# Kernel tuning notes

Measured on AMD Instinct MI355X. Metric: run time of the kernel, lower is better.

Reference implementation:

```python
import jax, jax.numpy as jnp
from jax import lax
import numpy as np

IOU_THR = 0.5
SCORE_THR = 0.0


def setup_inputs() -> dict:
    B, M, N, H, W = 8, 100, 32, 256, 256
    ks = jax.random.split(jax.random.key(0), 7)
    pxy = jax.random.uniform(ks[0], (B, M, 2), minval=0.0, maxval=512.0)
    pwh = jax.random.uniform(ks[1], (B, M, 2), minval=16.0, maxval=160.0)
    gxy = jax.random.uniform(ks[2], (B, N, 2), minval=0.0, maxval=512.0)
    gwh = jax.random.uniform(ks[3], (B, N, 2), minval=16.0, maxval=160.0)
    return {
        "pred_boxes": jnp.concatenate([pxy, pxy + pwh], axis=-1),  # xyxy
        "gt_boxes": jnp.concatenate([gxy, gxy + gwh], axis=-1),    # xyxy
        "pred_scores": jax.random.uniform(ks[4], (B, M)),
        "pred_masks": jax.random.uniform(ks[5], (B, M, H, W)),
        "mask_score": jax.random.uniform(ks[6], (B, M)),
    }


def pairwise_iou(b1, b2):
    # b1: [M,4], b2: [N,4] in xyxy -> [M,N]
    area1 = (b1[:, 2] - b1[:, 0]) * (b1[:, 3] - b1[:, 1])
    area2 = (b2[:, 2] - b2[:, 0]) * (b2[:, 3] - b2[:, 1])
    lt = jnp.maximum(b1[:, None, :2], b2[None, :, :2])
    rb = jnp.minimum(b1[:, None, 2:], b2[None, :, 2:])
    wh = jnp.clip(rb - lt, 0.0)
    inter = wh[..., 0] * wh[..., 1]
    return inter / (area1[:, None] + area2[None, :] - inter)


def _greedy_match(iou, scores):
    # iou: [M,N], scores: [M] -> gtm: [N] int32, biou: [N]
    N = iou.shape[1]
    order = jnp.argsort(-scores)  # descending score order

    def step(carry, i):
        gtm, biou = carry
        row = iou[i]
        # faithful to original: gt j is available if gtm[j] <= 0 (NOT > -1)
        cand = jnp.where((gtm <= 0) & (row >= IOU_THR), row, -1.0)
        m = jnp.argmax(cand)
        mx = cand[m]
        do = (scores[i] >= SCORE_THR) & (mx >= IOU_THR)
        gtm = jnp.where(do, gtm.at[m].set(i.astype(jnp.int32)), gtm)
        biou = jnp.where(do, biou.at[m].set(mx), biou)
        return (gtm, biou), None

    init = (jnp.full((N,), -1, jnp.int32), jnp.zeros((N,), iou.dtype))
    (gtm, biou), _ = lax.scan(step, init, order)
    return gtm, biou


def reference(pred_boxes, gt_boxes, pred_scores, pred_masks, mask_score):
    # per-image IoU matrices: [B,M,N]
    iou = jax.vmap(pairwise_iou)(pred_boxes, gt_boxes)
    gtm, biou = jax.vmap(_greedy_match)(iou, pred_scores)  # [B,N]
    matched = gtm > -1                                      # [B,N]
    idx = jnp.clip(gtm, 0)                                  # safe gather indices
    gathered = jax.vmap(lambda m, i: m[i])(pred_masks, idx)  # [B,N,H,W]
    gt_masks = jnp.where(matched[:, :, None, None], gathered, 0.0)
    flags = jnp.where(matched, jnp.take_along_axis(mask_score, idx, axis=1), 0.0)
    return gt_masks, flags, gtm, biou
```

## Files before the change

### kernel.cpp

```cpp
#include <hip/hip_runtime.h>
#include <hip/hip_bf16.h>

#define BB 8
#define MM 100
#define NN 32
#define HWSZ 65536
#define IOU_THR 0.5f
#define SCORE_THR 0.0f

#define MASKS_ELEMS ((size_t)BB * NN * HWSZ)

#define WS_FLAG 256

typedef unsigned int u32x4 __attribute__((ext_vector_type(4)));

__device__ __forceinline__ float bf16r(float x) {
    unsigned u = __float_as_uint(x);
    u = (u + 0x7FFFu + ((u >> 16) & 1u)) & 0xFFFF0000u;
    return __uint_as_float(u);
}

__global__ __launch_bounds__(256) void match_kernel(
    const void* __restrict__ pred_boxes,
    const void* __restrict__ gt_boxes,
    const void* __restrict__ pred_scores,
    const void* __restrict__ mask_score,
    void* __restrict__ out,
    int* __restrict__ ws)
{
    const int b = blockIdx.x;
    const int t = threadIdx.x;

    __shared__ float pb[MM][4];
    __shared__ float gb[NN][4];
    __shared__ float sc[MM];
    __shared__ float area2[NN];
    __shared__ float iou_s[MM][NN];
    __shared__ int   order_s[MM];
    __shared__ int   flag_s;

    if (t < 64) {
        const unsigned* gt_raw = (const unsigned*)gt_boxes;
        int cnt = 0;
        #pragma unroll
        for (int k = 0; k < 8; ++k) {
            const unsigned u  = gt_raw[t * 8 + k];
            const unsigned lo = u & 0xFFFFu;
            const unsigned ex = (lo >> 7) & 0xFFu;
            if (((lo >> 15) == 0u) && ex >= 118u && ex <= 137u) ++cnt;
        }
        #pragma unroll
        for (int m = 1; m < 64; m <<= 1) cnt += __shfl_xor(cnt, m, 64);
        if (t == 0) {
            flag_s = (cnt >= 256) ? 1 : 0;
            if (b == 0) ws[WS_FLAG] = flag_s;
        }
    }
    __syncthreads();
    const bool isbf = (flag_s != 0);

    const __hip_bfloat16* pb_h = (const __hip_bfloat16*)pred_boxes;
    const float*          pb_f = (const float*)pred_boxes;
    const __hip_bfloat16* gb_h = (const __hip_bfloat16*)gt_boxes;
    const float*          gb_f = (const float*)gt_boxes;
    const __hip_bfloat16* sc_h = (const __hip_bfloat16*)pred_scores;
    const float*          sc_f = (const float*)pred_scores;

    for (int i = t; i < MM * 4; i += 256) {
        const size_t o = (size_t)b * MM * 4 + i;
        pb[i >> 2][i & 3] = isbf ? __bfloat162float(pb_h[o]) : pb_f[o];
    }
    for (int i = t; i < NN * 4; i += 256) {
        const size_t o = (size_t)b * NN * 4 + i;
        gb[i >> 2][i & 3] = isbf ? __bfloat162float(gb_h[o]) : gb_f[o];
    }
    for (int i = t; i < MM; i += 256) {
        const size_t o = (size_t)b * MM + i;
        sc[i] = isbf ? __bfloat162float(sc_h[o]) : sc_f[o];
    }
    __syncthreads();

    auto rnd = [&](float x) { return isbf ? bf16r(x) : x; };

    if (t < NN)
        area2[t] = rnd(rnd(gb[t][2] - gb[t][0]) * rnd(gb[t][3] - gb[t][1]));
    __syncthreads();

    for (int e = t; e < MM * NN; e += 256) {
        const int i = e >> 5;
        const int j = e & 31;
        const float a1 = rnd(rnd(pb[i][2] - pb[i][0]) * rnd(pb[i][3] - pb[i][1]));
        const float lx = fmaxf(pb[i][0], gb[j][0]);
        const float ly = fmaxf(pb[i][1], gb[j][1]);
        const float rx = fminf(pb[i][2], gb[j][2]);
        const float ry = fminf(pb[i][3], gb[j][3]);
        const float w  = fmaxf(rnd(rx - lx), 0.0f);
        const float h  = fmaxf(rnd(ry - ly), 0.0f);
        const float inter = rnd(w * h);
        const float denom = rnd(rnd(a1 + area2[j]) - inter);
        iou_s[i][j] = rnd(inter / denom);
    }

    if (t < MM) {
        const float si = sc[t];
        int r = 0;
        for (int j = 0; j < MM; ++j) {
            const float sj = sc[j];
            if (sj > si || (sj == si && j < t)) ++r;
        }
        order_s[r] = t;
    }
    __syncthreads();

    if (t < 32) {
        const int j = t;
        int   gtm_j  = -1;
        float biou_j = 0.0f;

        for (int s = 0; s < MM; ++s) {
            const int i = order_s[s];
            const float row = iou_s[i][j];
            const float cand = (gtm_j <= 0 && row >= IOU_THR) ? row : -1.0f;

            float v  = cand;
            int   vj = j;
            #pragma unroll
            for (int m = 1; m < 32; m <<= 1) {
                const float ov = __shfl_xor(v, m, 32);
                const int   oj = __shfl_xor(vj, m, 32);
                if (ov > v || (ov == v && oj < vj)) { v = ov; vj = oj; }
            }
            const bool doit = (sc[i] >= SCORE_THR) && (v >= IOU_THR);
            if (doit && vj == j) { gtm_j = i; biou_j = v; }
        }

        const int bn = b * NN + j;
        const bool matched = (gtm_j > -1);
        float fs = 0.0f;
        if (matched) {
            const size_t o = (size_t)b * MM + gtm_j;
            fs = isbf ? __bfloat162float(((const __hip_bfloat16*)mask_score)[o])
                      : ((const float*)mask_score)[o];
        }
        if (isbf) {
            __hip_bfloat16* o = (__hip_bfloat16*)out;
            o[MASKS_ELEMS + bn]       = __float2bfloat16(fs);
            o[MASKS_ELEMS + 256 + bn] = __float2bfloat16((float)gtm_j);
            o[MASKS_ELEMS + 512 + bn] = __float2bfloat16(biou_j);
        } else {
            float* o = (float*)out;
            o[MASKS_ELEMS + bn]       = fs;
            o[MASKS_ELEMS + 256 + bn] = (float)gtm_j;
            o[MASKS_ELEMS + 512 + bn] = biou_j;
        }
        ws[bn] = gtm_j;
    }
}

#define CHUNK_BYTES 32768
#define CHUNKS_PER_MASK 8

__global__ __launch_bounds__(256) void gather_kernel(
    const void* __restrict__ pred_masks,
    const int* __restrict__ ws,
    void* __restrict__ out)
{
    const bool isbf = (ws[WS_FLAG] != 0);
    const int bn    = blockIdx.x >> 3;
    const int chunk = blockIdx.x & 7;
    const size_t mbytes = isbf ? (size_t)HWSZ * 2 : (size_t)HWSZ * 4;

    const size_t cbase = (size_t)chunk * CHUNK_BYTES;
    if (cbase >= mbytes) return;

    const int idx = ws[bn];
    const int b   = bn >> 5;

    const size_t tb = cbase + (size_t)threadIdx.x * 16;
    char* dst = (char*)out + (size_t)bn * mbytes;

    if (idx > -1) {
        const char* src = (const char*)pred_masks + ((size_t)b * MM + idx) * mbytes;
        u32x4 v[8];
        #pragma unroll
        for (int k = 0; k < 8; ++k)
            v[k] = __builtin_nontemporal_load((const u32x4*)(src + tb + (size_t)k * 4096));
        #pragma unroll
        for (int k = 0; k < 8; ++k)
            __builtin_nontemporal_store(v[k], (u32x4*)(dst + tb + (size_t)k * 4096));
    } else {
        const u32x4 z = (u32x4)0;
        #pragma unroll
        for (int k = 0; k < 8; ++k)
            __builtin_nontemporal_store(z, (u32x4*)(dst + tb + (size_t)k * 4096));
    }
}

extern "C" void kernel_launch(void* const* d_in, const int* in_sizes, int n_in,
                              void* d_out, int out_size, void* d_ws, size_t ws_size,
                              hipStream_t stream) {
    const void* pred_boxes  = d_in[0];
    const void* gt_boxes    = d_in[1];
    const void* pred_scores = d_in[2];
    const void* pred_masks  = d_in[3];
    const void* mask_score  = d_in[4];
    int* ws = (int*)d_ws;

    match_kernel<<<BB, 256, 0, stream>>>(pred_boxes, gt_boxes, pred_scores,
                                         mask_score, d_out, ws);
    gather_kernel<<<BB * NN * CHUNKS_PER_MASK, 256, 0, stream>>>(pred_masks, ws, d_out);
}
```

Baseline: 322.7 us.

## Fuse matching and mask gather into one kernel with redundant per-block matching

After: 372.3 us. 1.15x slower.

```diff
diff --git a/kernel.cpp b/kernel.cpp
--- a/kernel.cpp
+++ b/kernel.cpp
@@ -10,9 +10,10 @@
 
 #define MASKS_ELEMS ((size_t)BB * NN * HWSZ)
 
-#define WS_FLAG 256
-
 typedef unsigned int u32x4 __attribute__((ext_vector_type(4)));
+
+#define CHUNK_BYTES 32768
+#define CHUNKS_PER_MASK 8
 
 __device__ __forceinline__ float bf16r(float x) {
     unsigned u = __float_as_uint(x);
@@ -20,16 +21,20 @@
     return __uint_as_float(u);
 }
 
-__global__ __launch_bounds__(256) void match_kernel(
+__global__ __launch_bounds__(256) void fused_kernel(
     const void* __restrict__ pred_boxes,
     const void* __restrict__ gt_boxes,
     const void* __restrict__ pred_scores,
+    const void* __restrict__ pred_masks,
     const void* __restrict__ mask_score,
-    void* __restrict__ out,
-    int* __restrict__ ws)
+    void* __restrict__ out)
 {
-    const int b = blockIdx.x;
-    const int t = threadIdx.x;
+    const int bid   = blockIdx.x;
+    const int bn    = bid >> 3;
+    const int chunk = bid & 7;
+    const int b     = bn >> 5;
+    const int n     = bn & 31;
+    const int t     = threadIdx.x;
 
     __shared__ float pb[MM][4];
     __shared__ float gb[NN][4];
@@ -37,6 +42,7 @@
     __shared__ float area2[NN];
     __shared__ float iou_s[MM][NN];
     __shared__ int   order_s[MM];
+    __shared__ int   gtm_lds[NN];
     __shared__ int   flag_s;
 
     if (t < 64) {
@@ -51,13 +57,14 @@
         }
         #pragma unroll
         for (int m = 1; m < 64; m <<= 1) cnt += __shfl_xor(cnt, m, 64);
-        if (t == 0) {
-            flag_s = (cnt >= 256) ? 1 : 0;
-            if (b == 0) ws[WS_FLAG] = flag_s;
-        }
+        if (t == 0) flag_s = (cnt >= 256) ? 1 : 0;
     }
     __syncthreads();
     const bool isbf = (flag_s != 0);
+
+    const size_t mbytes = isbf ? (size_t)HWSZ * 2 : (size_t)HWSZ * 4;
+    const size_t cbase  = (size_t)chunk * CHUNK_BYTES;
+    if (cbase >= mbytes) return;
 
     const __hip_bfloat16* pb_h = (const __hip_bfloat16*)pred_boxes;
     const float*          pb_f = (const float*)pred_boxes;
@@ -134,49 +141,34 @@
             if (doit && vj == j) { gtm_j = i; biou_j = v; }
         }
 
-        const int bn = b * NN + j;
-        const bool matched = (gtm_j > -1);
-        float fs = 0.0f;
-        if (matched) {
-            const size_t o = (size_t)b * MM + gtm_j;
-            fs = isbf ? __bfloat162float(((const __hip_bfloat16*)mask_score)[o])
-                      : ((const float*)mask_score)[o];
-        }
-        if (isbf) {
-            __hip_bfloat16* o = (__hip_bfloat16*)out;
-            o[MASKS_ELEMS + bn]       = __float2bfloat16(fs);
-            o[MASKS_ELEMS + 256 + bn] = __float2bfloat16((float)gtm_j);
-            o[MASKS_ELEMS + 512 + bn] = __float2bfloat16(biou_j);
-        } else {
-            float* o = (float*)out;
-            o[MASKS_ELEMS + bn]       = fs;
-            o[MASKS_ELEMS + 256 + bn] = (float)gtm_j;
-            o[MASKS_ELEMS + 512 + bn] = biou_j;
-        }
-        ws[bn] = gtm_j;
-    }
-}
-
-#define CHUNK_BYTES 32768
-#define CHUNKS_PER_MASK 8
-
-__global__ __launch_bounds__(256) void gather_kernel(
-    const void* __restrict__ pred_masks,
-    const int* __restrict__ ws,
-    void* __restrict__ out)
-{
-    const bool isbf = (ws[WS_FLAG] != 0);
-    const int bn    = blockIdx.x >> 3;
-    const int chunk = blockIdx.x & 7;
-    const size_t mbytes = isbf ? (size_t)HWSZ * 2 : (size_t)HWSZ * 4;
-
-    const size_t cbase = (size_t)chunk * CHUNK_BYTES;
-    if (cbase >= mbytes) return;
-
-    const int idx = ws[bn];
-    const int b   = bn >> 5;
-
-    const size_t tb = cbase + (size_t)threadIdx.x * 16;
+        gtm_lds[j] = gtm_j;
+
+        if (chunk == 0 && j == n) {
+            const int obn = b * NN + j;
+            const bool matched = (gtm_j > -1);
+            float fs = 0.0f;
+            if (matched) {
+                const size_t o = (size_t)b * MM + gtm_j;
+                fs = isbf ? __bfloat162float(((const __hip_bfloat16*)mask_score)[o])
+                          : ((const float*)mask_score)[o];
+            }
+            if (isbf) {
+                __hip_bfloat16* o = (__hip_bfloat16*)out;
+                o[MASKS_ELEMS + obn]       = __float2bfloat16(fs);
+                o[MASKS_ELEMS + 256 + obn] = __float2bfloat16((float)gtm_j);
+                o[MASKS_ELEMS + 512 + obn] = __float2bfloat16(biou_j);
+            } else {
+                float* o = (float*)out;
+                o[MASKS_ELEMS + obn]       = fs;
+                o[MASKS_ELEMS + 256 + obn] = (float)gtm_j;
+                o[MASKS_ELEMS + 512 + obn] = biou_j;
+            }
+        }
+    }
+    __syncthreads();
+
+    const int idx = gtm_lds[n];
+    const size_t tb = cbase + (size_t)t * 16;
     char* dst = (char*)out + (size_t)bn * mbytes;
 
     if (idx > -1) {
@@ -204,9 +196,8 @@
     const void* pred_scores = d_in[2];
     const void* pred_masks  = d_in[3];
     const void* mask_score  = d_in[4];
-    int* ws = (int*)d_ws;
-
-    match_kernel<<<BB, 256, 0, stream>>>(pred_boxes, gt_boxes, pred_scores,
-                                         mask_score, d_out, ws);
-    gather_kernel<<<BB * NN * CHUNKS_PER_MASK, 256, 0, stream>>>(pred_masks, ws, d_out);
+    (void)d_ws; (void)ws_size;
+
+    fused_kernel<<<BB * NN * CHUNKS_PER_MASK, 256, 0, stream>>>(
+        pred_boxes, gt_boxes, pred_scores, pred_masks, mask_score, d_out);
 }
```

## Pack IoU and index into sortable keys and skip rows with no candidates

Applied to the files above, without the earlier changes.

Result: faster. 276.5 us (-14.3%).

```diff
diff --git a/kernel.cpp b/kernel.cpp
--- a/kernel.cpp
+++ b/kernel.cpp
@@ -31,13 +31,18 @@
     const int b = blockIdx.x;
     const int t = threadIdx.x;
 
-    __shared__ float pb[MM][4];
-    __shared__ float gb[NN][4];
-    __shared__ float sc[MM];
-    __shared__ float area2[NN];
-    __shared__ float iou_s[MM][NN];
-    __shared__ int   order_s[MM];
-    __shared__ int   flag_s;
+    __shared__ float    pb[MM][4];
+    __shared__ float    gb[NN][4];
+    __shared__ float    sc[MM];
+    __shared__ float    area2[NN];
+    __shared__ unsigned key_s[MM][NN];
+    __shared__ int      order_s[MM];
+    __shared__ int      rowflag[MM];
+    __shared__ int      clist[MM];
+    __shared__ int      ordc[MM];
+    __shared__ float    scoc[MM];
+    __shared__ int      cnt_s;
+    __shared__ int      flag_s;
 
     if (t < 64) {
         const unsigned* gt_raw = (const unsigned*)gt_boxes;
@@ -84,11 +89,22 @@
 
     if (t < NN)
         area2[t] = rnd(rnd(gb[t][2] - gb[t][0]) * rnd(gb[t][3] - gb[t][1]));
+
+    if (t < MM) {
+        const float si = sc[t];
+        int r = 0;
+        for (int j = 0; j < MM; ++j) {
+            const float sj = sc[j];
+            if (sj > si || (sj == si && j < t)) ++r;
+        }
+        order_s[r] = t;
+    }
     __syncthreads();
 
     for (int e = t; e < MM * NN; e += 256) {
-        const int i = e >> 5;
+        const int s = e >> 5;
         const int j = e & 31;
+        const int i = order_s[s];
         const float a1 = rnd(rnd(pb[i][2] - pb[i][0]) * rnd(pb[i][3] - pb[i][1]));
         const float lx = fmaxf(pb[i][0], gb[j][0]);
         const float ly = fmaxf(pb[i][1], gb[j][1]);
@@ -98,17 +114,27 @@
         const float h  = fmaxf(rnd(ry - ly), 0.0f);
         const float inter = rnd(w * h);
         const float denom = rnd(rnd(a1 + area2[j]) - inter);
-        iou_s[i][j] = rnd(inter / denom);
-    }
+        const float iou   = rnd(inter / denom);
+        unsigned key = 0u;
+        if (iou >= IOU_THR)
+            key = ((__float_as_uint(iou) - 0x3F000000u) << 6) | (32u - (unsigned)j);
+        key_s[s][j] = key;
+        const unsigned long long m = __ballot(key != 0u);
+        if (j == 0)
+            rowflag[s] = ((unsigned)(m >> (t & 32)) != 0u) ? 1 : 0;
+    }
+    __syncthreads();
 
     if (t < MM) {
-        const float si = sc[t];
         int r = 0;
-        for (int j = 0; j < MM; ++j) {
-            const float sj = sc[j];
-            if (sj > si || (sj == si && j < t)) ++r;
-        }
-        order_s[r] = t;
+        for (int u = 0; u < t; ++u) r += rowflag[u];
+        if (rowflag[t]) {
+            clist[r] = t;
+            const int i = order_s[t];
+            ordc[r] = i;
+            scoc[r] = sc[i];
+        }
+        if (t == MM - 1) cnt_s = r + rowflag[t];
     }
     __syncthreads();
 
@@ -116,22 +142,22 @@
         const int j = t;
         int   gtm_j  = -1;
         float biou_j = 0.0f;
-
-        for (int s = 0; s < MM; ++s) {
-            const int i = order_s[s];
-            const float row = iou_s[i][j];
-            const float cand = (gtm_j <= 0 && row >= IOU_THR) ? row : -1.0f;
-
-            float v  = cand;
-            int   vj = j;
+        const int cnt = cnt_s;
+
+        for (int p = 0; p < cnt; ++p) {
+            const int s = clist[p];
+            const unsigned key = key_s[s][j];
+            unsigned k = (gtm_j <= 0) ? key : 0u;
+            unsigned v = k;
             #pragma unroll
             for (int m = 1; m < 32; m <<= 1) {
-                const float ov = __shfl_xor(v, m, 32);
-                const int   oj = __shfl_xor(vj, m, 32);
-                if (ov > v || (ov == v && oj < vj)) { v = ov; vj = oj; }
+                const unsigned ov = __shfl_xor(v, m, 32);
+                v = (ov > v) ? ov : v;
             }
-            const bool doit = (sc[i] >= SCORE_THR) && (v >= IOU_THR);
-            if (doit && vj == j) { gtm_j = i; biou_j = v; }
+            if (v != 0u && scoc[p] >= SCORE_THR && k == v) {
+                gtm_j  = ordc[p];
+                biou_j = __uint_as_float((v >> 6) + 0x3F000000u);
+            }
         }
 
         const int bn = b * NN + j;
```
